# Performance work log

Hardware: AMD Instinct MI355X
Metric: run time of the kernel (lower is better)

## Reference

```python
import jax, jax.numpy as jnp
import numpy as np

N, L, E, H = 4, 4096, 1024, 1024


def setup_inputs() -> dict:
    key = jax.random.key(0)
    ks = jax.random.split(key, 7)
    s_in = 1.0 / np.sqrt(E)
    return {
        "X_embed": jax.random.normal(ks[0], (N, L, E), dtype=jnp.float32),
        "Wq": jax.random.normal(ks[1], (H, E), dtype=jnp.float32) * s_in,
        "bq": jnp.zeros((H,), dtype=jnp.float32),
        "Wk": jax.random.normal(ks[2], (H, E), dtype=jnp.float32) * s_in,
        "bk": jnp.zeros((H,), dtype=jnp.float32),
        "Wv": jax.random.normal(ks[3], (H, E), dtype=jnp.float32) * s_in,
        "bv": jnp.zeros((H,), dtype=jnp.float32),
    }


def reference(X_embed, Wq, bq, Wk, bk, Wv, bv):
    # Linear projections: (N, L, E) @ (E, H) + (H,) -> (N, L, H)
    Q = jnp.einsum('nle,he->nlh', X_embed, Wq) + bq
    K = jnp.einsum('nle,he->nlh', X_embed, Wk) + bk
    V = jnp.einsum('nle,he->nlh', X_embed, Wv) + bv
    # Scores (N, L, L); original scales by sqrt(Out.shape[2]) == sqrt(L)
    S = jnp.einsum('nah,nbh->nab', Q, K) / jnp.asarray(np.sqrt(float(L)), dtype=Q.dtype)
    # Original softmax is over dim=1 (the query axis 'a')
    A = jax.nn.softmax(S, axis=1)
    # 'nll,nlh->nlh': diagonal of A times V, elementwise over h
    diag = jnp.diagonal(A, axis1=1, axis2=2)  # (N, L)
    return diag[:, :, None] * V
```

## Files before the change

kernel.cpp:

```cpp
#include <hip/hip_runtime.h>
#include <hip/hip_bf16.h>
#include <stdint.h>

#define NB 4
#define LS 4096
#define ED 1024
#define HD 1024
#define MR (NB * LS)
#define SCALE_S (1.0f / 64.0f)

typedef __attribute__((ext_vector_type(8))) short bf16x8;
typedef __attribute__((ext_vector_type(8))) int   i32x8;
typedef __attribute__((ext_vector_type(4))) float f32x4;

__device__ __forceinline__ unsigned short f2bf(float f) {
    union { float f; uint32_t u; } x; x.f = f;
    uint32_t r = x.u + 0x7fffu + ((x.u >> 16) & 1u);
    return (unsigned short)(r >> 16);
}

__device__ __forceinline__ void load_lds16(const void* g, void* s) {
    __builtin_amdgcn_global_load_lds(
        (const __attribute__((address_space(1))) void*)g,
        (__attribute__((address_space(3))) void*)s, 16, 0, 0);
}

#define XCHUNKS (MR * ED / 4)
#define WCHUNKS (3 * ED * ED / 4)
__global__ void __launch_bounds__(256) cast_all_k(
    const float4* __restrict__ X, const float4* __restrict__ wq,
    const float4* __restrict__ wk, const float4* __restrict__ wv,
    ushort4* __restrict__ Xb, ushort4* __restrict__ Wall)
{
    const int i = blockIdx.x * 256 + threadIdx.x;
    if (i < XCHUNKS) {
        const float4 v = X[i];
        ushort4 o; o.x = f2bf(v.x); o.y = f2bf(v.y); o.z = f2bf(v.z); o.w = f2bf(v.w);
        Xb[i] = o;
    } else if (i < XCHUNKS + WCHUNKS) {
        const int j = i - XCHUNKS;
        const int s = j >> 18, jj = j & 0x3ffff;
        const float4 v = (s == 0 ? wq : s == 1 ? wk : wv)[jj];
        ushort4 o; o.x = f2bf(v.x); o.y = f2bf(v.y); o.z = f2bf(v.z); o.w = f2bf(v.w);
        Wall[j] = o;
    }
}

#define QK_BAR() do { asm volatile("" ::: "memory"); \
    __builtin_amdgcn_s_barrier(); asm volatile("" ::: "memory"); } while (0)
#define PH_MID() do { QK_BAR(); \
    asm volatile("s_waitcnt lgkmcnt(0)" ::: "memory"); \
    __builtin_amdgcn_sched_barrier(0); \
    __builtin_amdgcn_s_setprio(1); } while (0)
#define PH_END() do { __builtin_amdgcn_s_setprio(0); QK_BAR(); } while (0)
#define PH_END_VM6() do { __builtin_amdgcn_s_setprio(0); \
    asm volatile("s_waitcnt vmcnt(6)" ::: "memory"); QK_BAR(); } while (0)
#define PH_END_VM0() do { __builtin_amdgcn_s_setprio(0); \
    asm volatile("s_waitcnt vmcnt(0)" ::: "memory"); QK_BAR(); } while (0)

__device__ __forceinline__ void read_af(bf16x8 (&af)[4][2], const char* base,
                                        int arow, int sw7, int quad) {
#pragma unroll
    for (int mf = 0; mf < 4; mf++) {
        const char* r = base + (arow + mf * 16) * 128;
        af[mf][0] = *(const bf16x8*)(r + ((quad * 16) ^ sw7));
        af[mf][1] = *(const bf16x8*)(r + ((64 + quad * 16) ^ sw7));
    }
}
__device__ __forceinline__ void read_wf(bf16x8 (&wf)[4], const char* base,
                                        int wrow, int ks64, int sw7, int quad) {
#pragma unroll
    for (int nf = 0; nf < 4; nf++)
        wf[nf] = *(const bf16x8*)(base + (wrow + nf * 16) * 128 + ((ks64 + quad * 16) ^ sw7));
}
template<int KS>
__device__ __forceinline__ void mfma16(f32x4 (&acc)[4][4], const bf16x8 (&af)[4][2],
                                       const bf16x8 (&wf)[4]) {
#pragma unroll
    for (int mf = 0; mf < 4; mf++)
#pragma unroll
        for (int nf = 0; nf < 4; nf++)
            acc[mf][nf] = __builtin_amdgcn_mfma_f32_16x16x32_bf16(
                wf[nf], af[mf][KS], acc[mf][nf], 0, 0, 0);
}

__global__ void __launch_bounds__(512) __attribute__((amdgpu_waves_per_eu(2, 2)))
gemm_qk_fused8(const unsigned short* __restrict__ A,
               const unsigned short* __restrict__ W,
               const float* __restrict__ bq, const float* __restrict__ bk,
               unsigned char* __restrict__ Qf8t, unsigned char* __restrict__ Kf8t,
               float* __restrict__ diag)
{
    extern __shared__ char lds[];
    const int t = threadIdx.x;
    const int w = t >> 6, lane = t & 63, quad = lane >> 4, l16 = lane & 15;
    const int wm = w >> 1, wn = w & 1;

    const int swz = (blockIdx.x & 7) * 64 + (blockIdx.x >> 3);
    const long blockM = (long)(swz >> 3) * 256;
    const int  blockN = (swz & 7) * 128;

    const long srow = (long)(w * 8 + (lane >> 3)) * 2048
                    + (long)(((lane & 7) ^ (lane >> 3)) << 4);
    const char* gA  = (const char*)A + blockM * 2048 + srow;
    const char* gAh = gA + 128 * 2048;
    const char* gWq = (const char*)W + (long)blockN * 2048 + srow;
    const char* gWk = gWq + (long)1024 * 2048;
    char* dst = lds + w * 1024;

#define ST(G, OFF, KB) do { \
    load_lds16((G) + (KB), dst + (OFF)); \
    load_lds16((G) + 131072 + (KB), dst + (OFF) + 8192); } while (0)

    const char* A0 = lds;          const char* A1 = lds + 65536;
    const char* Q0 = lds + 32768;  const char* Q1 = lds + 65536 + 32768;
    const char* K0 = lds + 49152;  const char* K1 = lds + 65536 + 49152;

    const int arow = wm * 64 + l16;
    const int wrow = wn * 64 + l16;
    const int sw7  = (l16 & 7) << 4;

    f32x4 aq[4][4] = {}; f32x4 ak[4][4] = {};
    bf16x8 aF[4][2], wF[4];

    ST(gA, 0, 0); ST(gAh, 16384, 0); ST(gWq, 32768, 0); ST(gWk, 49152, 0);
    ST(gA, 65536, 128); ST(gAh, 65536 + 16384, 128); ST(gWq, 65536 + 32768, 128);
    asm volatile("s_waitcnt vmcnt(6)" ::: "memory");
    QK_BAR();

#pragma unroll 1
    for (int i = 0; i < 7; ++i) {
        const long k1 = (2L * i + 1) * 128, k2 = (2L * i + 2) * 128, k3 = (2L * i + 3) * 128;
        read_af(aF, A0, arow, sw7, quad);
        read_wf(wF, Q0, wrow, 0, sw7, quad);
        ST(gWk, 65536 + 49152, k1);
        asm volatile("s_waitcnt lgkmcnt(8)" ::: "memory");
        PH_MID(); mfma16<0>(aq, aF, wF); PH_END();
        read_wf(wF, Q0, wrow, 64, sw7, quad);
        ST(gA, 0, k2);
        PH_MID(); mfma16<1>(aq, aF, wF); PH_END();
        read_wf(wF, K0, wrow, 0, sw7, quad);
        ST(gAh, 16384, k2);
        PH_MID(); mfma16<0>(ak, aF, wF); PH_END();
        read_wf(wF, K0, wrow, 64, sw7, quad);
        ST(gWq, 32768, k2);
        PH_MID(); mfma16<1>(ak, aF, wF); PH_END_VM6();
        read_af(aF, A1, arow, sw7, quad);
        read_wf(wF, Q1, wrow, 0, sw7, quad);
        ST(gWk, 49152, k2);
        asm volatile("s_waitcnt lgkmcnt(8)" ::: "memory");
        PH_MID(); mfma16<0>(aq, aF, wF); PH_END();
        read_wf(wF, Q1, wrow, 64, sw7, quad);
        ST(gA, 65536, k3);
        PH_MID(); mfma16<1>(aq, aF, wF); PH_END();
        read_wf(wF, K1, wrow, 0, sw7, quad);
        ST(gAh, 65536 + 16384, k3);
        PH_MID(); mfma16<0>(ak, aF, wF); PH_END();
        read_wf(wF, K1, wrow, 64, sw7, quad);
        ST(gWq, 65536 + 32768, k3);
        PH_MID(); mfma16<1>(ak, aF, wF); PH_END_VM6();
    }
    {
        read_af(aF, A0, arow, sw7, quad);
        read_wf(wF, Q0, wrow, 0, sw7, quad);
        ST(gWk, 65536 + 49152, 15L * 128);
        asm volatile("s_waitcnt lgkmcnt(8)" ::: "memory");
        PH_MID(); mfma16<0>(aq, aF, wF); PH_END();
        read_wf(wF, Q0, wrow, 64, sw7, quad);
        PH_MID(); mfma16<1>(aq, aF, wF); PH_END();
        read_wf(wF, K0, wrow, 0, sw7, quad);
        PH_MID(); mfma16<0>(ak, aF, wF); PH_END();
        read_wf(wF, K0, wrow, 64, sw7, quad);
        PH_MID(); mfma16<1>(ak, aF, wF); PH_END_VM0();
        read_af(aF, A1, arow, sw7, quad);
        read_wf(wF, Q1, wrow, 0, sw7, quad);
        PH_MID(); mfma16<0>(aq, aF, wF); PH_END();
        read_wf(wF, Q1, wrow, 64, sw7, quad);
        PH_MID(); mfma16<1>(aq, aF, wF); PH_END();
        read_wf(wF, K1, wrow, 0, sw7, quad);
        PH_MID(); mfma16<0>(ak, aF, wF); PH_END();
        read_wf(wF, K1, wrow, 64, sw7, quad);
        PH_MID(); mfma16<1>(ak, aF, wF); PH_END();
    }
#undef ST

    float dp[4] = {0.f, 0.f, 0.f, 0.f};
#pragma unroll
    for (int nf = 0; nf < 4; nf++) {
        const int col = blockN + wn * 64 + nf * 16 + quad * 4;
        const float4 q4 = *(const float4*)(bq + col);
        const float4 k4 = *(const float4*)(bk + col);
#pragma unroll
        for (int mf = 0; mf < 4; mf++) {
            const size_t row = (size_t)(blockM + wm * 64 + mf * 16 + l16);
            const float vq0 = aq[mf][nf][0] + q4.x, vq1 = aq[mf][nf][1] + q4.y;
            const float vq2 = aq[mf][nf][2] + q4.z, vq3 = aq[mf][nf][3] + q4.w;
            const float vk0 = ak[mf][nf][0] + k4.x, vk1 = ak[mf][nf][1] + k4.y;
            const float vk2 = ak[mf][nf][2] + k4.z, vk3 = ak[mf][nf][3] + k4.w;
            uint32_t uq = 0, uk = 0;
            uq = __builtin_amdgcn_cvt_pk_fp8_f32(vq0, vq1, uq, false);
            uq = __builtin_amdgcn_cvt_pk_fp8_f32(vq2, vq3, uq, true);
            uk = __builtin_amdgcn_cvt_pk_fp8_f32(vk0, vk1, uk, false);
            uk = __builtin_amdgcn_cvt_pk_fp8_f32(vk2, vk3, uk, true);
            const size_t f8 = (row >> 4) * 16384 + (size_t)(col >> 4) * 256
                            + (row & 15) * 16 + (col & 15);
            *(uint32_t*)(Qf8t + f8) = uq;
            *(uint32_t*)(Kf8t + f8) = uk;
            dp[mf] += vq0 * vk0 + vq1 * vk1 + vq2 * vk2 + vq3 * vk3;
        }
    }
#pragma unroll
    for (int mf = 0; mf < 4; mf++) {
        float d = dp[mf];
        d += __shfl_xor(d, 16);
        d += __shfl_xor(d, 32);
        if (quad == 0)
            atomicAdd(&diag[blockM + wm * 64 + mf * 16 + l16], d);
    }
}

__global__ void __launch_bounds__(256)
gemm_f8_denom(const unsigned char* __restrict__ Qt,
              const unsigned char* __restrict__ Kt,
              float* __restrict__ denom)
{
    __shared__ __align__(16) unsigned char As[16384];
    __shared__ __align__(16) unsigned char Bs[16384];

    const int t = threadIdx.x;
    const int wid = t >> 6, lane = t & 63, quad = lane >> 4, l16 = lane & 15;
    const int m0 = (wid >> 1) * 64, n0 = (wid & 1) * 64;
    const size_t zoff = (size_t)blockIdx.z * LS * (size_t)HD;
    const unsigned char* A = Qt + zoff;
    const unsigned char* B = Kt + zoff;
    float* dn = denom + (size_t)blockIdx.z * LS;
    const int blockM = blockIdx.y * 128;
    const int blockN = blockIdx.x * 128;

    size_t aoff[4], boff[4];
#pragma unroll
    for (int j = 0; j < 4; j++) {
        const int iw = wid * 4 + j;
        const size_t lo = (size_t)((iw & 1) * 4 + (lane >> 4)) * 256 + (size_t)(lane & 15) * 16;
        aoff[j] = ((size_t)(blockM >> 4) + (iw >> 1)) * 16384 + lo;
        boff[j] = ((size_t)(blockN >> 4) + (iw >> 1)) * 16384 + lo;
    }

    f32x4 acc[4][4] = {};

    for (int kt = 0; kt < 8; kt++) {
        const size_t ko = (size_t)kt * 2048;
#pragma unroll
        for (int j = 0; j < 4; j++) {
            load_lds16(A + aoff[j] + ko, (char*)As + (wid * 4 + j) * 1024);
            load_lds16(B + boff[j] + ko, (char*)Bs + (wid * 4 + j) * 1024);
        }
        __syncthreads();

        i32x8 aF[4], bF[4];
#pragma unroll
        for (int mf = 0; mf < 4; mf++) {
            const int base = (((m0 >> 4) + mf) * 2048) + quad * 512 + l16 * 16;
            const int4 lo = *(const int4*)(As + base);
            const int4 hi = *(const int4*)(As + base + 256);
            aF[mf][0] = lo.x; aF[mf][1] = lo.y; aF[mf][2] = lo.z; aF[mf][3] = lo.w;
            aF[mf][4] = hi.x; aF[mf][5] = hi.y; aF[mf][6] = hi.z; aF[mf][7] = hi.w;
        }
#pragma unroll
        for (int nf = 0; nf < 4; nf++) {
            const int base = (((n0 >> 4) + nf) * 2048) + quad * 512 + l16 * 16;
            const int4 lo = *(const int4*)(Bs + base);
            const int4 hi = *(const int4*)(Bs + base + 256);
            bF[nf][0] = lo.x; bF[nf][1] = lo.y; bF[nf][2] = lo.z; bF[nf][3] = lo.w;
            bF[nf][4] = hi.x; bF[nf][5] = hi.y; bF[nf][6] = hi.z; bF[nf][7] = hi.w;
        }
#pragma unroll
        for (int mf = 0; mf < 4; mf++)
#pragma unroll
            for (int nf = 0; nf < 4; nf++)
                acc[mf][nf] = __builtin_amdgcn_mfma_scale_f32_16x16x128_f8f6f4(
                    aF[mf], bF[nf], acc[mf][nf],
                    0, 0,
                    0, 0x7f7f7f7f,
                    0, 0x7f7f7f7f);
        __syncthreads();
    }

#pragma unroll
    for (int nf = 0; nf < 4; nf++) {
        float s = 0.f;
#pragma unroll
        for (int mf = 0; mf < 4; mf++)
#pragma unroll
            for (int r = 0; r < 4; r++)
                s += __expf(acc[mf][nf][r] * SCALE_S);
        s += __shfl_xor(s, 16);
        s += __shfl_xor(s, 32);
        if (quad == 0)
            atomicAdd(&dn[blockN + n0 + nf * 16 + l16], s);
    }
}

__global__ void __launch_bounds__(512)
gemm_v8fin(const unsigned short* __restrict__ A,
           const unsigned short* __restrict__ Wv,
           const float* __restrict__ bv, const float* __restrict__ diag,
           const float* __restrict__ denom, float* __restrict__ out)
{
    extern __shared__ char lds[];
    const int t = threadIdx.x;
    const int w = t >> 6, lane = t & 63, quad = lane >> 4, l16 = lane & 15;
    const int wm = w >> 1, wn = w & 1;

    const int swz = (blockIdx.x & 7) * 64 + (blockIdx.x >> 3);
    const long blockM = (long)(swz >> 3) * 256;
    const int  blockN = (swz & 7) * 128;

    const int scol = (((t & 3) ^ ((t >> 2) & 3)) << 4);
    const char* gA0 = (const char*)A + (blockM + (t >> 2)) * 2048 + scol;
    const char* gA1 = gA0 + 128 * 2048;
    const char* gW0 = (const char*)Wv + ((long)blockN + (t >> 2)) * 2048 + scol;

    const int arow = wm * 64 + l16;
    const int wrow = wn * 64 + l16;
    const int rdoff = (quad * 16) ^ ((l16 & 3) << 4);

    f32x4 acc[4][4] = {};
    bf16x8 aF[4], wF[4];

#define VBA(J) (lds + (J) * 24576)
#define VST(J, KT) do { \
    load_lds16(gA0 + (long)(KT) * 64, VBA(J) + w * 1024); \
    load_lds16(gA1 + (long)(KT) * 64, VBA(J) + 8192 + w * 1024); \
    load_lds16(gW0 + (long)(KT) * 64, VBA(J) + 16384 + w * 1024); } while (0)
#define VREAD(J) do { \
    const char* Ab_ = VBA(J); const char* Wb_ = VBA(J) + 16384; \
    _Pragma("unroll") for (int mf = 0; mf < 4; mf++) \
        aF[mf] = *(const bf16x8*)(Ab_ + (arow + mf * 16) * 64 + rdoff); \
    _Pragma("unroll") for (int nf = 0; nf < 4; nf++) \
        wF[nf] = *(const bf16x8*)(Wb_ + (wrow + nf * 16) * 64 + rdoff); } while (0)
#define VCOMP() do { \
    asm volatile("s_waitcnt lgkmcnt(0)" ::: "memory"); \
    __builtin_amdgcn_sched_barrier(0); \
    __builtin_amdgcn_s_setprio(1); \
    _Pragma("unroll") for (int mf = 0; mf < 4; mf++) \
    _Pragma("unroll") for (int nf = 0; nf < 4; nf++) \
        acc[mf][nf] = __builtin_amdgcn_mfma_f32_16x16x32_bf16( \
            wF[nf], aF[mf], acc[mf][nf], 0, 0, 0); \
    __builtin_amdgcn_s_setprio(0); } while (0)
#define VEND3() do { asm volatile("s_waitcnt vmcnt(3)" ::: "memory"); QK_BAR(); } while (0)

    VST(0, 0); VST(1, 1);
    asm volatile("s_waitcnt vmcnt(3)" ::: "memory");
    QK_BAR();

#pragma unroll 1
    for (int i = 0; i < 10; ++i) {
        const int b = 3 * i;
        VREAD(0); VST(2, b + 2); VCOMP(); VEND3();
        VREAD(1); VST(0, b + 3); VCOMP(); VEND3();
        VREAD(2); VST(1, b + 4); VCOMP(); VEND3();
    }
    VREAD(0); VCOMP();
    asm volatile("s_waitcnt vmcnt(0)" ::: "memory"); QK_BAR();
    VREAD(1); VCOMP();
#undef VBA
#undef VST
#undef VREAD
#undef VCOMP
#undef VEND3

#pragma unroll
    for (int mf = 0; mf < 4; mf++) {
        const long row = blockM + wm * 64 + mf * 16 + l16;
        const float sc = __expf(diag[row] * SCALE_S) / denom[row];
#pragma unroll
        for (int nf = 0; nf < 4; nf++) {
            const int col = blockN + wn * 64 + nf * 16 + quad * 4;
            const float4 b4 = *(const float4*)(bv + col);
            float4 o;
            o.x = (acc[mf][nf][0] + b4.x) * sc;
            o.y = (acc[mf][nf][1] + b4.y) * sc;
            o.z = (acc[mf][nf][2] + b4.z) * sc;
            o.w = (acc[mf][nf][3] + b4.w) * sc;
            *(float4*)(out + row * 1024 + col) = o;
        }
    }
}

extern "C" void kernel_launch(void* const* d_in, const int* in_sizes, int n_in,
                              void* d_out, int out_size, void* d_ws, size_t ws_size,
                              hipStream_t stream)
{
    (void)in_sizes; (void)n_in; (void)out_size; (void)ws_size;
    const float* X  = (const float*)d_in[0];
    const float* Wq = (const float*)d_in[1];
    const float* bq = (const float*)d_in[2];
    const float* Wk = (const float*)d_in[3];
    const float* bk = (const float*)d_in[4];
    const float* Wv = (const float*)d_in[5];
    const float* bv = (const float*)d_in[6];
    float* out = (float*)d_out;

    char* p = (char*)d_ws;
    unsigned short* Xb   = (unsigned short*)p; p += (size_t)MR * ED * 2;
    unsigned short* Wall = (unsigned short*)p; p += (size_t)3072 * ED * 2;
    unsigned char*  Qf8t = (unsigned char*)p;  p += (size_t)MR * HD;
    unsigned char*  Kf8t = (unsigned char*)p;  p += (size_t)MR * HD;
    float* diag  = (float*)p; p += (size_t)MR * 4;
    float* denom = (float*)p; p += (size_t)MR * 4;

    dim3 blk(256);

    static int init8 = 0;
    if (!init8) {
        hipFuncSetAttribute((const void*)gemm_qk_fused8,
                            hipFuncAttributeMaxDynamicSharedMemorySize, 131072);
        hipFuncSetAttribute((const void*)gemm_v8fin,
                            hipFuncAttributeMaxDynamicSharedMemorySize, 73728);
        init8 = 1;
    }

    cast_all_k<<<(XCHUNKS + WCHUNKS + 255) / 256, blk, 0, stream>>>(
        (const float4*)X, (const float4*)Wq, (const float4*)Wk, (const float4*)Wv,
        (ushort4*)Xb, (ushort4*)Wall);

    hipMemsetAsync(diag, 0, 2 * MR * sizeof(float), stream);

    gemm_qk_fused8<<<dim3(512), dim3(512), 131072, stream>>>(
        Xb, Wall, bq, bk, Qf8t, Kf8t, diag);

    dim3 gden(LS / 128, LS / 128, NB);
    gemm_f8_denom<<<gden, blk, 0, stream>>>(Qf8t, Kf8t, denom);

    gemm_v8fin<<<dim3(512), dim3(512), 73728, stream>>>(
        Xb, Wall + (size_t)2048 * ED, bv, diag, denom, out);
}
```

Before: 313.5 us.

## Rewrite FP8 denominator GEMM with triple-buffered LDS pipeline and larger tiles

Replaces the 128x128 single-buffered FP8 score/denominator GEMM with a 512-thread kernel computing 128x256 tiles. It uses three LDS stages with asynchronous global-to-LDS loads, explicit waitcnt and barriers, MFMA priority hints, and split B-fragment reads. Block indices are swizzled across XCDs for L2 locality. The aim is to hide global load latency behind MFMA work and cut per-tile load overhead, at the cost of 144KB LDS per block, which limits occupancy.

Result: slower. 331.3 us (+5.7%).

```diff
diff --git a/kernel.cpp b/kernel.cpp
--- a/kernel.cpp
+++ b/kernel.cpp
@@ -219,73 +219,95 @@
     }
 }
 
-__global__ void __launch_bounds__(256)
-gemm_f8_denom(const unsigned char* __restrict__ Qt,
-              const unsigned char* __restrict__ Kt,
-              float* __restrict__ denom)
+__device__ __forceinline__ void read_f8(i32x8 &f, const char* p) {
+    const int4 lo = *(const int4*)p;
+    const int4 hi = *(const int4*)(p + 256);
+    f[0] = lo.x; f[1] = lo.y; f[2] = lo.z; f[3] = lo.w;
+    f[4] = hi.x; f[5] = hi.y; f[6] = hi.z; f[7] = hi.w;
+}
+
+__global__ void __launch_bounds__(512)
+gemm_f8_denomp(const unsigned char* __restrict__ Qt,
+               const unsigned char* __restrict__ Kt,
+               float* __restrict__ denom)
 {
-    __shared__ __align__(16) unsigned char As[16384];
-    __shared__ __align__(16) unsigned char Bs[16384];
-
+    extern __shared__ char lds[];
     const int t = threadIdx.x;
-    const int wid = t >> 6, lane = t & 63, quad = lane >> 4, l16 = lane & 15;
-    const int m0 = (wid >> 1) * 64, n0 = (wid & 1) * 64;
-    const size_t zoff = (size_t)blockIdx.z * LS * (size_t)HD;
-    const unsigned char* A = Qt + zoff;
-    const unsigned char* B = Kt + zoff;
-    float* dn = denom + (size_t)blockIdx.z * LS;
-    const int blockM = blockIdx.y * 128;
-    const int blockN = blockIdx.x * 128;
-
-    size_t aoff[4], boff[4];
-#pragma unroll
-    for (int j = 0; j < 4; j++) {
-        const int iw = wid * 4 + j;
-        const size_t lo = (size_t)((iw & 1) * 4 + (lane >> 4)) * 256 + (size_t)(lane & 15) * 16;
-        aoff[j] = ((size_t)(blockM >> 4) + (iw >> 1)) * 16384 + lo;
-        boff[j] = ((size_t)(blockN >> 4) + (iw >> 1)) * 16384 + lo;
-    }
+    const int w = t >> 6, lane = t & 63, quad = lane >> 4, l16 = lane & 15;
+    const int wm = w >> 2, wn = w & 3;
+
+    const int pos = (blockIdx.x & 7) * 256 + (blockIdx.x >> 3);
+    const int z = pos >> 9;
+    const int rem = pos & 511;
+    const int blockM = (rem >> 4) * 128;
+    const int blockN = (rem & 15) * 256;
+
+    const size_t zoff = (size_t)z * LS * (size_t)HD;
+    const long stg = (long)(t >> 7) * 16384 + (long)(t & 127) * 16;
+    const unsigned char* gA = Qt + zoff + (size_t)(blockM >> 4) * 16384 + stg;
+    const unsigned char* gB = Kt + zoff + (size_t)(blockN >> 4) * 16384 + stg;
+
+#define DBUF(J) (lds + (J) * 49152)
+#define DST(J, KT) do { \
+    load_lds16(gA +          (long)(KT) * 2048, DBUF(J) +         w * 1024); \
+    load_lds16(gA + 65536  + (long)(KT) * 2048, DBUF(J) + 8192  + w * 1024); \
+    load_lds16(gB +          (long)(KT) * 2048, DBUF(J) + 16384 + w * 1024); \
+    load_lds16(gB + 65536  + (long)(KT) * 2048, DBUF(J) + 24576 + w * 1024); \
+    load_lds16(gB + 131072 + (long)(KT) * 2048, DBUF(J) + 32768 + w * 1024); \
+    load_lds16(gB + 196608 + (long)(KT) * 2048, DBUF(J) + 40960 + w * 1024); } while (0)
+
+    const int abase = (wm * 4) * 2048 + quad * 512 + l16 * 16;
+    const int bbase = 16384 + (wn * 4) * 2048 + quad * 512 + l16 * 16;
 
     f32x4 acc[4][4] = {};
-
-    for (int kt = 0; kt < 8; kt++) {
-        const size_t ko = (size_t)kt * 2048;
-#pragma unroll
-        for (int j = 0; j < 4; j++) {
-            load_lds16(A + aoff[j] + ko, (char*)As + (wid * 4 + j) * 1024);
-            load_lds16(B + boff[j] + ko, (char*)Bs + (wid * 4 + j) * 1024);
-        }
-        __syncthreads();
-
-        i32x8 aF[4], bF[4];
-#pragma unroll
-        for (int mf = 0; mf < 4; mf++) {
-            const int base = (((m0 >> 4) + mf) * 2048) + quad * 512 + l16 * 16;
-            const int4 lo = *(const int4*)(As + base);
-            const int4 hi = *(const int4*)(As + base + 256);
-            aF[mf][0] = lo.x; aF[mf][1] = lo.y; aF[mf][2] = lo.z; aF[mf][3] = lo.w;
-            aF[mf][4] = hi.x; aF[mf][5] = hi.y; aF[mf][6] = hi.z; aF[mf][7] = hi.w;
-        }
-#pragma unroll
-        for (int nf = 0; nf < 4; nf++) {
-            const int base = (((n0 >> 4) + nf) * 2048) + quad * 512 + l16 * 16;
-            const int4 lo = *(const int4*)(Bs + base);
-            const int4 hi = *(const int4*)(Bs + base + 256);
-            bF[nf][0] = lo.x; bF[nf][1] = lo.y; bF[nf][2] = lo.z; bF[nf][3] = lo.w;
-            bF[nf][4] = hi.x; bF[nf][5] = hi.y; bF[nf][6] = hi.z; bF[nf][7] = hi.w;
-        }
-#pragma unroll
-        for (int mf = 0; mf < 4; mf++)
-#pragma unroll
-            for (int nf = 0; nf < 4; nf++)
-                acc[mf][nf] = __builtin_amdgcn_mfma_scale_f32_16x16x128_f8f6f4(
-                    aF[mf], bF[nf], acc[mf][nf],
-                    0, 0,
-                    0, 0x7f7f7f7f,
-                    0, 0x7f7f7f7f);
-        __syncthreads();
-    }
-
+    i32x8 aF[4], bF[2];
+
+#define DMFMA(NF, BI) \
+    acc[mf][NF] = __builtin_amdgcn_mfma_scale_f32_16x16x128_f8f6f4( \
+        aF[mf], bF[BI], acc[mf][NF], 0, 0, 0, 0x7f7f7f7f, 0, 0x7f7f7f7f)
+
+#define DTILE(J, STG, ENDW) do { \
+    const char* Db_ = DBUF(J); \
+    read_f8(aF[0], Db_ + abase);        read_f8(aF[1], Db_ + abase + 2048); \
+    read_f8(aF[2], Db_ + abase + 4096); read_f8(aF[3], Db_ + abase + 6144); \
+    read_f8(bF[0], Db_ + bbase);        read_f8(bF[1], Db_ + bbase + 2048); \
+    STG; \
+    asm volatile("s_waitcnt lgkmcnt(0)" ::: "memory"); \
+    __builtin_amdgcn_sched_barrier(0); \
+    __builtin_amdgcn_s_setprio(1); \
+    _Pragma("unroll") for (int mf = 0; mf < 4; mf++) { DMFMA(0, 0); DMFMA(1, 1); } \
+    __builtin_amdgcn_s_setprio(0); \
+    read_f8(bF[0], Db_ + bbase + 4096); read_f8(bF[1], Db_ + bbase + 6144); \
+    asm volatile("s_waitcnt lgkmcnt(0)" ::: "memory"); \
+    __builtin_amdgcn_sched_barrier(0); \
+    __builtin_amdgcn_s_setprio(1); \
+    _Pragma("unroll") for (int mf = 0; mf < 4; mf++) { DMFMA(2, 0); DMFMA(3, 1); } \
+    __builtin_amdgcn_s_setprio(0); \
+    ENDW; \
+} while (0)
+
+#define DEND6() do { asm volatile("s_waitcnt vmcnt(6)" ::: "memory"); QK_BAR(); } while (0)
+
+    DST(0, 0); DST(1, 1);
+    asm volatile("s_waitcnt vmcnt(6)" ::: "memory");
+    QK_BAR();
+
+#pragma unroll 1
+    for (int i = 0; i < 2; ++i) {
+        const int b = 3 * i;
+        DTILE(0, DST(2, b + 2), DEND6());
+        DTILE(1, DST(0, b + 3), DEND6());
+        DTILE(2, DST(1, b + 4), DEND6());
+    }
+    DTILE(0, (void)0, { asm volatile("s_waitcnt vmcnt(0)" ::: "memory"); QK_BAR(); });
+    DTILE(1, (void)0, (void)0);
+#undef DBUF
+#undef DST
+#undef DMFMA
+#undef DTILE
+#undef DEND6
+
+    float* dn = denom + (size_t)z * LS;
 #pragma unroll
     for (int nf = 0; nf < 4; nf++) {
         float s = 0.f;
@@ -297,7 +319,7 @@
         s += __shfl_xor(s, 16);
         s += __shfl_xor(s, 32);
         if (quad == 0)
-            atomicAdd(&dn[blockN + n0 + nf * 16 + l16], s);
+            atomicAdd(&dn[blockN + wn * 64 + nf * 16 + l16], s);
     }
 }
 
@@ -416,6 +438,8 @@
     if (!init8) {
         hipFuncSetAttribute((const void*)gemm_qk_fused8,
                             hipFuncAttributeMaxDynamicSharedMemorySize, 131072);
+        hipFuncSetAttribute((const void*)gemm_f8_denomp,
+                            hipFuncAttributeMaxDynamicSharedMemorySize, 147456);
         hipFuncSetAttribute((const void*)gemm_v8fin,
                             hipFuncAttributeMaxDynamicSharedMemorySize, 73728);
         init8 = 1;
@@ -430,8 +454,7 @@
     gemm_qk_fused8<<<dim3(512), dim3(512), 131072, stream>>>(
         Xb, Wall, bq, bk, Qf8t, Kf8t, diag);
 
-    dim3 gden(LS / 128, LS / 128, NB);
-    gemm_f8_denom<<<gden, blk, 0, stream>>>(Qf8t, Kf8t, denom);
+    gemm_f8_denomp<<<dim3(2048), dim3(512), 147456, stream>>>(Qf8t, Kf8t, denom);
 
     gemm_v8fin<<<dim3(512), dim3(512), 73728, stream>>>(
         Xb, Wall + (size_t)2048 * ED, bv, diag, denom, out);
```

## Replace fused QK GEMM with simpler double-buffered kernel and pipeline denom GEMM

Applied to the files above, without the earlier changes.

Replaces the hand-scheduled 512-thread, 256x128-tile QK projection kernel with a simpler 256-thread, 128x128-tile kernel. The new kernel uses a 32-wide K step and double-buffered LDS without swizzling. The FP8 denominator GEMM also gets double-buffered LDS, so the next K tile is prefetched while the current one is multiplied, replacing the two syncthreads per iteration. The aim is to overlap global loads with MFMA work and raise occupancy. The trade-off is that the unswizzled LDS reads may hit bank conflicts, and the smaller tiles lower data reuse compared with the carefully scheduled original.

Result: slower. 409.8 us (+30.7%).

```diff
diff --git a/kernel.cpp b/kernel.cpp
--- a/kernel.cpp
+++ b/kernel.cpp
@@ -48,155 +48,106 @@
 
 #define QK_BAR() do { asm volatile("" ::: "memory"); \
     __builtin_amdgcn_s_barrier(); asm volatile("" ::: "memory"); } while (0)
-#define PH_MID() do { QK_BAR(); \
+#define LGKM0_PRIO() do { \
     asm volatile("s_waitcnt lgkmcnt(0)" ::: "memory"); \
     __builtin_amdgcn_sched_barrier(0); \
     __builtin_amdgcn_s_setprio(1); } while (0)
-#define PH_END() do { __builtin_amdgcn_s_setprio(0); QK_BAR(); } while (0)
-#define PH_END_VM6() do { __builtin_amdgcn_s_setprio(0); \
-    asm volatile("s_waitcnt vmcnt(6)" ::: "memory"); QK_BAR(); } while (0)
-#define PH_END_VM0() do { __builtin_amdgcn_s_setprio(0); \
-    asm volatile("s_waitcnt vmcnt(0)" ::: "memory"); QK_BAR(); } while (0)
-
-__device__ __forceinline__ void read_af(bf16x8 (&af)[4][2], const char* base,
-                                        int arow, int sw7, int quad) {
-#pragma unroll
-    for (int mf = 0; mf < 4; mf++) {
-        const char* r = base + (arow + mf * 16) * 128;
-        af[mf][0] = *(const bf16x8*)(r + ((quad * 16) ^ sw7));
-        af[mf][1] = *(const bf16x8*)(r + ((64 + quad * 16) ^ sw7));
-    }
-}
-__device__ __forceinline__ void read_wf(bf16x8 (&wf)[4], const char* base,
-                                        int wrow, int ks64, int sw7, int quad) {
-#pragma unroll
-    for (int nf = 0; nf < 4; nf++)
-        wf[nf] = *(const bf16x8*)(base + (wrow + nf * 16) * 128 + ((ks64 + quad * 16) ^ sw7));
-}
-template<int KS>
-__device__ __forceinline__ void mfma16(f32x4 (&acc)[4][4], const bf16x8 (&af)[4][2],
-                                       const bf16x8 (&wf)[4]) {
-#pragma unroll
-    for (int mf = 0; mf < 4; mf++)
+#define PRIO_OFF() __builtin_amdgcn_s_setprio(0)
+#define TILE_END() do { asm volatile("s_waitcnt vmcnt(0)" ::: "memory"); QK_BAR(); } while (0)
+
+__global__ void __launch_bounds__(256)
+gemm_qk4(const unsigned short* __restrict__ A,
+         const unsigned short* __restrict__ W,
+         const float* __restrict__ bq, const float* __restrict__ bk,
+         unsigned char* __restrict__ Qf8t, unsigned char* __restrict__ Kf8t,
+         float* __restrict__ diag)
+{
+    __shared__ __align__(16) unsigned short As[2][4096];
+    __shared__ __align__(16) unsigned short Ws0[2][4096];
+    __shared__ __align__(16) unsigned short Ws1[2][4096];
+
+    const int t = threadIdx.x;
+    const int wid = t >> 6, lane = t & 63, quad = lane >> 4, l16 = lane & 15;
+    const int m0 = (wid >> 1) * 64, n0 = (wid & 1) * 64;
+    const long blockM = (long)blockIdx.y * 128;
+    const int blockN = blockIdx.x * 128;
+
+    const char* a_g  = (const char*)(A + (blockM + (t >> 2)) * (size_t)ED + (size_t)((t & 3) * 8));
+    const char* w0_g = (const char*)(W + ((size_t)blockN + (t >> 2)) * ED + (size_t)((t & 3) * 8));
+    const char* w1_g = w0_g + (size_t)1024 * ED * 2;
+    const size_t half = (size_t)64 * ED * 2;
+    const int dstoff = wid * 1024;
+
+#define QSTG(BUF, KT) do { \
+    const int kb_ = (KT) * 64; \
+    load_lds16(a_g  + kb_,        (char*)As[BUF]  + dstoff); \
+    load_lds16(a_g  + kb_ + half, (char*)As[BUF]  + dstoff + 4096); \
+    load_lds16(w0_g + kb_,        (char*)Ws0[BUF] + dstoff); \
+    load_lds16(w0_g + kb_ + half, (char*)Ws0[BUF] + dstoff + 4096); \
+    load_lds16(w1_g + kb_,        (char*)Ws1[BUF] + dstoff); \
+    load_lds16(w1_g + kb_ + half, (char*)Ws1[BUF] + dstoff + 4096); } while (0)
+
+    f32x4 acc[2][4][4] = {};
+
+    QSTG(0, 0);
+    asm volatile("s_waitcnt vmcnt(0)" ::: "memory");
+    QK_BAR();
+
+    int buf = 0;
+#pragma unroll 1
+    for (int kt = 0; kt < 32; ++kt) {
+        if (kt < 31) QSTG(buf ^ 1, kt + 1);
+
+        bf16x8 aF[4], bF[4];
+        const char* AsB = (const char*)As[buf];
+#pragma unroll
+        for (int mf = 0; mf < 4; mf++)
+            aF[mf] = *(const bf16x8*)(AsB + ((m0 + mf * 16 + l16) * 32 + quad * 8) * 2);
+
+        const char* W0B = (const char*)Ws0[buf];
 #pragma unroll
         for (int nf = 0; nf < 4; nf++)
-            acc[mf][nf] = __builtin_amdgcn_mfma_f32_16x16x32_bf16(
-                wf[nf], af[mf][KS], acc[mf][nf], 0, 0, 0);
-}
-
-__global__ void __launch_bounds__(512) __attribute__((amdgpu_waves_per_eu(2, 2)))
-gemm_qk_fused8(const unsigned short* __restrict__ A,
-               const unsigned short* __restrict__ W,
-               const float* __restrict__ bq, const float* __restrict__ bk,
-               unsigned char* __restrict__ Qf8t, unsigned char* __restrict__ Kf8t,
-               float* __restrict__ diag)
-{
-    extern __shared__ char lds[];
-    const int t = threadIdx.x;
-    const int w = t >> 6, lane = t & 63, quad = lane >> 4, l16 = lane & 15;
-    const int wm = w >> 1, wn = w & 1;
-
-    const int swz = (blockIdx.x & 7) * 64 + (blockIdx.x >> 3);
-    const long blockM = (long)(swz >> 3) * 256;
-    const int  blockN = (swz & 7) * 128;
-
-    const long srow = (long)(w * 8 + (lane >> 3)) * 2048
-                    + (long)(((lane & 7) ^ (lane >> 3)) << 4);
-    const char* gA  = (const char*)A + blockM * 2048 + srow;
-    const char* gAh = gA + 128 * 2048;
-    const char* gWq = (const char*)W + (long)blockN * 2048 + srow;
-    const char* gWk = gWq + (long)1024 * 2048;
-    char* dst = lds + w * 1024;
-
-#define ST(G, OFF, KB) do { \
-    load_lds16((G) + (KB), dst + (OFF)); \
-    load_lds16((G) + 131072 + (KB), dst + (OFF) + 8192); } while (0)
-
-    const char* A0 = lds;          const char* A1 = lds + 65536;
-    const char* Q0 = lds + 32768;  const char* Q1 = lds + 65536 + 32768;
-    const char* K0 = lds + 49152;  const char* K1 = lds + 65536 + 49152;
-
-    const int arow = wm * 64 + l16;
-    const int wrow = wn * 64 + l16;
-    const int sw7  = (l16 & 7) << 4;
-
-    f32x4 aq[4][4] = {}; f32x4 ak[4][4] = {};
-    bf16x8 aF[4][2], wF[4];
-
-    ST(gA, 0, 0); ST(gAh, 16384, 0); ST(gWq, 32768, 0); ST(gWk, 49152, 0);
-    ST(gA, 65536, 128); ST(gAh, 65536 + 16384, 128); ST(gWq, 65536 + 32768, 128);
-    asm volatile("s_waitcnt vmcnt(6)" ::: "memory");
-    QK_BAR();
-
-#pragma unroll 1
-    for (int i = 0; i < 7; ++i) {
-        const long k1 = (2L * i + 1) * 128, k2 = (2L * i + 2) * 128, k3 = (2L * i + 3) * 128;
-        read_af(aF, A0, arow, sw7, quad);
-        read_wf(wF, Q0, wrow, 0, sw7, quad);
-        ST(gWk, 65536 + 49152, k1);
-        asm volatile("s_waitcnt lgkmcnt(8)" ::: "memory");
-        PH_MID(); mfma16<0>(aq, aF, wF); PH_END();
-        read_wf(wF, Q0, wrow, 64, sw7, quad);
-        ST(gA, 0, k2);
-        PH_MID(); mfma16<1>(aq, aF, wF); PH_END();
-        read_wf(wF, K0, wrow, 0, sw7, quad);
-        ST(gAh, 16384, k2);
-        PH_MID(); mfma16<0>(ak, aF, wF); PH_END();
-        read_wf(wF, K0, wrow, 64, sw7, quad);
-        ST(gWq, 32768, k2);
-        PH_MID(); mfma16<1>(ak, aF, wF); PH_END_VM6();
-        read_af(aF, A1, arow, sw7, quad);
-        read_wf(wF, Q1, wrow, 0, sw7, quad);
-        ST(gWk, 49152, k2);
-        asm volatile("s_waitcnt lgkmcnt(8)" ::: "memory");
-        PH_MID(); mfma16<0>(aq, aF, wF); PH_END();
-        read_wf(wF, Q1, wrow, 64, sw7, quad);
-        ST(gA, 65536, k3);
-        PH_MID(); mfma16<1>(aq, aF, wF); PH_END();
-        read_wf(wF, K1, wrow, 0, sw7, quad);
-        ST(gAh, 65536 + 16384, k3);
-        PH_MID(); mfma16<0>(ak, aF, wF); PH_END();
-        read_wf(wF, K1, wrow, 64, sw7, quad);
-        ST(gWq, 65536 + 32768, k3);
-        PH_MID(); mfma16<1>(ak, aF, wF); PH_END_VM6();
-    }
-    {
-        read_af(aF, A0, arow, sw7, quad);
-        read_wf(wF, Q0, wrow, 0, sw7, quad);
-        ST(gWk, 65536 + 49152, 15L * 128);
-        asm volatile("s_waitcnt lgkmcnt(8)" ::: "memory");
-        PH_MID(); mfma16<0>(aq, aF, wF); PH_END();
-        read_wf(wF, Q0, wrow, 64, sw7, quad);
-        PH_MID(); mfma16<1>(aq, aF, wF); PH_END();
-        read_wf(wF, K0, wrow, 0, sw7, quad);
-        PH_MID(); mfma16<0>(ak, aF, wF); PH_END();
-        read_wf(wF, K0, wrow, 64, sw7, quad);
-        PH_MID(); mfma16<1>(ak, aF, wF); PH_END_VM0();
-        read_af(aF, A1, arow, sw7, quad);
-        read_wf(wF, Q1, wrow, 0, sw7, quad);
-        PH_MID(); mfma16<0>(aq, aF, wF); PH_END();
-        read_wf(wF, Q1, wrow, 64, sw7, quad);
-        PH_MID(); mfma16<1>(aq, aF, wF); PH_END();
-        read_wf(wF, K1, wrow, 0, sw7, quad);
-        PH_MID(); mfma16<0>(ak, aF, wF); PH_END();
-        read_wf(wF, K1, wrow, 64, sw7, quad);
-        PH_MID(); mfma16<1>(ak, aF, wF); PH_END();
-    }
-#undef ST
+            bF[nf] = *(const bf16x8*)(W0B + ((n0 + nf * 16 + l16) * 32 + quad * 8) * 2);
+        LGKM0_PRIO();
+#pragma unroll
+        for (int mf = 0; mf < 4; mf++)
+#pragma unroll
+            for (int nf = 0; nf < 4; nf++)
+                acc[0][mf][nf] = __builtin_amdgcn_mfma_f32_16x16x32_bf16(
+                    bF[nf], aF[mf], acc[0][mf][nf], 0, 0, 0);
+        PRIO_OFF();
+
+        const char* W1B = (const char*)Ws1[buf];
+#pragma unroll
+        for (int nf = 0; nf < 4; nf++)
+            bF[nf] = *(const bf16x8*)(W1B + ((n0 + nf * 16 + l16) * 32 + quad * 8) * 2);
+        LGKM0_PRIO();
+#pragma unroll
+        for (int mf = 0; mf < 4; mf++)
+#pragma unroll
+            for (int nf = 0; nf < 4; nf++)
+                acc[1][mf][nf] = __builtin_amdgcn_mfma_f32_16x16x32_bf16(
+                    bF[nf], aF[mf], acc[1][mf][nf], 0, 0, 0);
+        PRIO_OFF();
+
+        TILE_END();
+        buf ^= 1;
+    }
+#undef QSTG
 
     float dp[4] = {0.f, 0.f, 0.f, 0.f};
 #pragma unroll
     for (int nf = 0; nf < 4; nf++) {
-        const int col = blockN + wn * 64 + nf * 16 + quad * 4;
+        const int col = blockN + n0 + nf * 16 + quad * 4;
         const float4 q4 = *(const float4*)(bq + col);
         const float4 k4 = *(const float4*)(bk + col);
 #pragma unroll
         for (int mf = 0; mf < 4; mf++) {
-            const size_t row = (size_t)(blockM + wm * 64 + mf * 16 + l16);
-            const float vq0 = aq[mf][nf][0] + q4.x, vq1 = aq[mf][nf][1] + q4.y;
-            const float vq2 = aq[mf][nf][2] + q4.z, vq3 = aq[mf][nf][3] + q4.w;
-            const float vk0 = ak[mf][nf][0] + k4.x, vk1 = ak[mf][nf][1] + k4.y;
-            const float vk2 = ak[mf][nf][2] + k4.z, vk3 = ak[mf][nf][3] + k4.w;
+            const size_t row = (size_t)(blockM + m0 + mf * 16 + l16);
+            const float vq0 = acc[0][mf][nf][0] + q4.x, vq1 = acc[0][mf][nf][1] + q4.y;
+            const float vq2 = acc[0][mf][nf][2] + q4.z, vq3 = acc[0][mf][nf][3] + q4.w;
+            const float vk0 = acc[1][mf][nf][0] + k4.x, vk1 = acc[1][mf][nf][1] + k4.y;
+            const float vk2 = acc[1][mf][nf][2] + k4.z, vk3 = acc[1][mf][nf][3] + k4.w;
             uint32_t uq = 0, uk = 0;
             uq = __builtin_amdgcn_cvt_pk_fp8_f32(vq0, vq1, uq, false);
             uq = __builtin_amdgcn_cvt_pk_fp8_f32(vq2, vq3, uq, true);
@@ -215,17 +166,24 @@
         d += __shfl_xor(d, 16);
         d += __shfl_xor(d, 32);
         if (quad == 0)
-            atomicAdd(&diag[blockM + wm * 64 + mf * 16 + l16], d);
-    }
+            atomicAdd(&diag[blockM + m0 + mf * 16 + l16], d);
+    }
+}
+
+__device__ __forceinline__ void read_f8(i32x8 &f, const char* p) {
+    const int4 lo = *(const int4*)p;
+    const int4 hi = *(const int4*)(p + 256);
+    f[0] = lo.x; f[1] = lo.y; f[2] = lo.z; f[3] = lo.w;
+    f[4] = hi.x; f[5] = hi.y; f[6] = hi.z; f[7] = hi.w;
 }
 
 __global__ void __launch_bounds__(256)
-gemm_f8_denom(const unsigned char* __restrict__ Qt,
+gemm_f8_den2b(const unsigned char* __restrict__ Qt,
               const unsigned char* __restrict__ Kt,
               float* __restrict__ denom)
 {
-    __shared__ __align__(16) unsigned char As[16384];
-    __shared__ __align__(16) unsigned char Bs[16384];
+    __shared__ __align__(16) unsigned char As[2][16384];
+    __shared__ __align__(16) unsigned char Bs[2][16384];
 
     const int t = threadIdx.x;
     const int wid = t >> 6, lane = t & 63, quad = lane >> 4, l16 = lane & 15;
@@ -246,34 +204,35 @@
         boff[j] = ((size_t)(blockN >> 4) + (iw >> 1)) * 16384 + lo;
     }
 
+#define DSTG(BUF, KT) do { \
+    const size_t ko_ = (size_t)(KT) * 2048; \
+    _Pragma("unroll") for (int j = 0; j < 4; j++) { \
+        load_lds16(A + aoff[j] + ko_, (char*)As[BUF] + (wid * 4 + j) * 1024); \
+        load_lds16(B + boff[j] + ko_, (char*)Bs[BUF] + (wid * 4 + j) * 1024); } } while (0)
+
     f32x4 acc[4][4] = {};
 
-    for (int kt = 0; kt < 8; kt++) {
-        const size_t ko = (size_t)kt * 2048;
-#pragma unroll
-        for (int j = 0; j < 4; j++) {
-            load_lds16(A + aoff[j] + ko, (char*)As + (wid * 4 + j) * 1024);
-            load_lds16(B + boff[j] + ko, (char*)Bs + (wid * 4 + j) * 1024);
-        }
-        __syncthreads();
+    DSTG(0, 0);
+    asm volatile("s_waitcnt vmcnt(0)" ::: "memory");
+    QK_BAR();
+
+    int buf = 0;
+#pragma unroll 1
+    for (int kt = 0; kt < 8; ++kt) {
+        if (kt < 7) DSTG(buf ^ 1, kt + 1);
 
         i32x8 aF[4], bF[4];
 #pragma unroll
         for (int mf = 0; mf < 4; mf++) {
             const int base = (((m0 >> 4) + mf) * 2048) + quad * 512 + l16 * 16;
-            const int4 lo = *(const int4*)(As + base);
-            const int4 hi = *(const int4*)(As + base + 256);
-            aF[mf][0] = lo.x; aF[mf][1] = lo.y; aF[mf][2] = lo.z; aF[mf][3] = lo.w;
-            aF[mf][4] = hi.x; aF[mf][5] = hi.y; aF[mf][6] = hi.z; aF[mf][7] = hi.w;
+            read_f8(aF[mf], (const char*)As[buf] + base);
         }
 #pragma unroll
         for (int nf = 0; nf < 4; nf++) {
             const int base = (((n0 >> 4) + nf) * 2048) + quad * 512 + l16 * 16;
-            const int4 lo = *(const int4*)(Bs + base);
-            const int4 hi = *(const int4*)(Bs + base + 256);
-            bF[nf][0] = lo.x; bF[nf][1] = lo.y; bF[nf][2] = lo.z; bF[nf][3] = lo.w;
-            bF[nf][4] = hi.x; bF[nf][5] = hi.y; bF[nf][6] = hi.z; bF[nf][7] = hi.w;
+            read_f8(bF[nf], (const char*)Bs[buf] + base);
         }
+        LGKM0_PRIO();
 #pragma unroll
         for (int mf = 0; mf < 4; mf++)
 #pragma unroll
@@ -283,8 +242,12 @@
                     0, 0,
                     0, 0x7f7f7f7f,
                     0, 0x7f7f7f7f);
-        __syncthreads();
-    }
+        PRIO_OFF();
+
+        TILE_END();
+        buf ^= 1;
+    }
+#undef DSTG
 
 #pragma unroll
     for (int nf = 0; nf < 4; nf++) {
@@ -414,8 +377,6 @@
 
     static int init8 = 0;
     if (!init8) {
-        hipFuncSetAttribute((const void*)gemm_qk_fused8,
-                            hipFuncAttributeMaxDynamicSharedMemorySize, 131072);
         hipFuncSetAttribute((const void*)gemm_v8fin,
                             hipFuncAttributeMaxDynamicSharedMemorySize, 73728);
         init8 = 1;
@@ -427,11 +388,11 @@
 
     hipMemsetAsync(diag, 0, 2 * MR * sizeof(float), stream);
 
-    gemm_qk_fused8<<<dim3(512), dim3(512), 131072, stream>>>(
-        Xb, Wall, bq, bk, Qf8t, Kf8t, diag);
+    dim3 gqk(HD / 128, MR / 128);
+    gemm_qk4<<<gqk, blk, 0, stream>>>(Xb, Wall, bq, bk, Qf8t, Kf8t, diag);
 
     dim3 gden(LS / 128, LS / 128, NB);
-    gemm_f8_denom<<<gden, blk, 0, stream>>>(Qf8t, Kf8t, denom);
+    gemm_f8_den2b<<<gden, blk, 0, stream>>>(Qf8t, Kf8t, denom);
 
     gemm_v8fin<<<dim3(512), dim3(512), 73728, stream>>>(
         Xb, Wall + (size_t)2048 * ED, bv, diag, denom, out);
```
